# Performance work log

Hardware: AMD Instinct MI355X
Metric: run time of the kernel (lower is better)

Reference implementation:

```python
import jax, jax.numpy as jnp
import numpy as np

N_NODES = 50000
N_EDGES = 800000
BATCH = 8
IN_CH = 64
OUT_CH = 64
K = 6


def setup_inputs() -> dict:
    key = jax.random.key(0)
    k1, k2, k3, k4 = jax.random.split(key, 4)
    x = jax.random.normal(k1, (BATCH, N_NODES, IN_CH), dtype=jnp.float32)
    edge_index = jax.random.randint(k2, (2, N_EDGES), 0, N_NODES, dtype=jnp.int64)
    # small weights keep the order-K Chebyshev recursion numerically stable
    edge_weight = jax.random.normal(k3, (N_EDGES,), dtype=jnp.float32) * 0.05
    W = jax.random.normal(k4, (K, IN_CH, OUT_CH), dtype=jnp.float32) * (1.0 / np.sqrt(IN_CH))
    bias = jnp.zeros((OUT_CH,), dtype=jnp.float32)
    return {"x": x, "edge_index": edge_index, "edge_weight": edge_weight, "W": W, "bias": bias}


def _spmm(edge_index, edge_weight, x, n_nodes):
    # sparse Laplacian @ x for batched features x: [B, N, C]
    src = edge_index[1]  # gather column
    dst = edge_index[0]  # scatter row
    msg = x[:, src, :] * edge_weight[None, :, None]      # [B, E, C]
    agg = jax.ops.segment_sum(msg.transpose(1, 0, 2), dst, num_segments=n_nodes)  # [N, B, C]
    return agg.transpose(1, 0, 2)                        # [B, N, C]


def reference(x, edge_index, edge_weight, W, bias):
    n = x.shape[1]
    t_prev = x                                            # T_0
    out = jnp.einsum('bnc,co->bno', t_prev, W[0])
    if K > 1:
        t_cur = _spmm(edge_index, edge_weight, x, n)      # T_1 = L x
        out = out + jnp.einsum('bnc,co->bno', t_cur, W[1])
        for k in range(2, K):
            t_next = 2.0 * _spmm(edge_index, edge_weight, t_cur, n) - t_prev
            out = out + jnp.einsum('bnc,co->bno', t_next, W[k])
            t_prev, t_cur = t_cur, t_next
    out = out + bias
    return out
```

## Files before the change

### kernel.cpp

```cpp
#include <hip/hip_runtime.h>

#define N_NODES 50000
#define N_EDGES 800000
#define BATCH 8
#define CH 64
#define BC (BATCH * CH)
#define WSZ (CH * CH)
#define NROWS (BATCH * N_NODES)
#define TELEMS ((size_t)NROWS * CH)

typedef unsigned short u16;
typedef short bf16x8 __attribute__((ext_vector_type(8)));
typedef float f32x4 __attribute__((ext_vector_type(4)));
typedef unsigned short u16x4 __attribute__((ext_vector_type(4)));
typedef unsigned short u16x8 __attribute__((ext_vector_type(8)));

__device__ __forceinline__ u16 f2bf(float f) {
    unsigned x = __float_as_uint(f);
    return (u16)((x + 0x7fffu + ((x >> 16) & 1u)) >> 16);
}
__device__ __forceinline__ float b2f(u16 u) {
    return __uint_as_float(((unsigned)u) << 16);
}


__global__ void hist_kernel(const int* __restrict__ dst, int* __restrict__ cursor, int E) {
    int e = blockIdx.x * blockDim.x + threadIdx.x;
    if (e < E) atomicAdd(&cursor[dst[e]], 1);
}

__global__ void scan_kernel(int* cursor, int* __restrict__ row_ptr, int n) {
    const int T = 1024;
    int tid = threadIdx.x;
    int per = (n + T - 1) / T;
    int s = tid * per;
    int e = s + per; if (e > n) e = n;
    int sum = 0;
    for (int i = s; i < e; ++i) sum += cursor[i];
    __shared__ int lds[1024];
    lds[tid] = sum;
    __syncthreads();
    for (int off = 1; off < 1024; off <<= 1) {
        int t = (tid >= off) ? lds[tid - off] : 0;
        __syncthreads();
        lds[tid] += t;
        __syncthreads();
    }
    int run = lds[tid] - sum;
    for (int i = s; i < e; ++i) {
        int v = cursor[i];
        row_ptr[i] = run;
        cursor[i]  = run;
        run += v;
    }
    if (tid == T - 1) row_ptr[n] = run;
}

__global__ void scatter_kernel(const int* __restrict__ dst, const int* __restrict__ src,
                               const float* __restrict__ w, int* cursor,
                               int2* __restrict__ edges, int E) {
    int e = blockIdx.x * blockDim.x + threadIdx.x;
    if (e >= E) return;
    int d = dst[e];
    int p = atomicAdd(&cursor[d], 1);
    edges[p] = make_int2(src[e], __float_as_int(w[e]));
}

__global__ __launch_bounds__(256) void cast_x(const float* __restrict__ x, u16* __restrict__ xb) {
    size_t i = (size_t)blockIdx.x * 256 + threadIdx.x;
    f32x4 v = __builtin_nontemporal_load((const f32x4*)(x + i * 4));
    int c4 = (int)(i & 15);
    size_t bn = i >> 4;
    int b = (int)(bn / N_NODES);
    int n = (int)(bn - (size_t)b * N_NODES);
    u16x4 o;
    o.x = f2bf(v.x); o.y = f2bf(v.y); o.z = f2bf(v.z); o.w = f2bf(v.w);
    *(u16x4*)(xb + ((size_t)n * BATCH + b) * CH + c4 * 4) = o;
}

__global__ __launch_bounds__(256) void pack_w(const float* __restrict__ W, u16* __restrict__ wpack) {
    int id = blockIdx.x * 256 + threadIdx.x;
    if (id >= 48 * 64) return;
    int lane = id & 63, frag = id >> 6;
    int ct = frag & 3, cct = (frag >> 2) & 1, k = frag >> 3;
    int m = lane & 15, quad = lane >> 4;
    int c = ct * 16 + m;
#pragma unroll
    for (int j = 0; j < 8; ++j) {
        int cc = cct * 32 + quad * 8 + j;
        wpack[(size_t)id * 8 + j] = f2bf(W[k * WSZ + cc * CH + c]);
    }
}

template <bool HAS_PREV>
__global__ __launch_bounds__(256) void spmm_kernel(
        const u16* __restrict__ tcur,
        const u16* __restrict__ tprev,
        u16* __restrict__ tnext,
        const int* __restrict__ row_ptr,
        const int2* __restrict__ edges) {
    const int nwaves = gridDim.x * 4;
    const int wid = blockIdx.x * 4 + (threadIdx.x >> 6);
    const int lane = threadIdx.x & 63;
    const size_t lo = (size_t)lane * 8;

    for (int node = wid; node < N_NODES; node += nwaves) {
        float acc[8];
#pragma unroll
        for (int q = 0; q < 8; ++q) acc[q] = 0.f;

        const int beg = row_ptr[node], end = row_ptr[node + 1];
        for (int e0 = beg; e0 < end; e0 += 64) {
            int m = end - e0; if (m > 64) m = 64;
            int2 ev = edges[e0 + (lane < m ? lane : 0)];
            for (int j = 0; j < m; j += 4) {
                int   s0 = __shfl(ev.x, j);
                float w0 = __int_as_float(__shfl(ev.y, j));
                int   j1 = (j + 1 < m) ? j + 1 : j;
                int   s1 = __shfl(ev.x, j1);
                float w1 = (j + 1 < m) ? __int_as_float(__shfl(ev.y, j1)) : 0.f;
                int   j2 = (j + 2 < m) ? j + 2 : j;
                int   s2 = __shfl(ev.x, j2);
                float w2 = (j + 2 < m) ? __int_as_float(__shfl(ev.y, j2)) : 0.f;
                int   j3 = (j + 3 < m) ? j + 3 : j;
                int   s3 = __shfl(ev.x, j3);
                float w3 = (j + 3 < m) ? __int_as_float(__shfl(ev.y, j3)) : 0.f;
                u16x8 v0 = *(const u16x8*)(tcur + (size_t)s0 * BC + lo);
                u16x8 v1 = *(const u16x8*)(tcur + (size_t)s1 * BC + lo);
                u16x8 v2 = *(const u16x8*)(tcur + (size_t)s2 * BC + lo);
                u16x8 v3 = *(const u16x8*)(tcur + (size_t)s3 * BC + lo);
#pragma unroll
                for (int q = 0; q < 8; ++q) acc[q] = fmaf(w0, b2f(v0[q]), acc[q]);
#pragma unroll
                for (int q = 0; q < 8; ++q) acc[q] = fmaf(w1, b2f(v1[q]), acc[q]);
#pragma unroll
                for (int q = 0; q < 8; ++q) acc[q] = fmaf(w2, b2f(v2[q]), acc[q]);
#pragma unroll
                for (int q = 0; q < 8; ++q) acc[q] = fmaf(w3, b2f(v3[q]), acc[q]);
            }
        }

        const size_t idx = (size_t)node * BC + lo;
        u16x8 o;
        if (HAS_PREV) {
            u16x8 pv = *(const u16x8*)(tprev + idx);
#pragma unroll
            for (int q = 0; q < 8; ++q) o[q] = f2bf(2.f * acc[q] - b2f(pv[q]));
        } else {
#pragma unroll
            for (int q = 0; q < 8; ++q) o[q] = f2bf(acc[q]);
        }
        *(u16x8*)(tnext + idx) = o;
    }
}

__global__ __launch_bounds__(256) void out_gemm(
        const u16* __restrict__ tbase, size_t tstride,
        const u16* __restrict__ wpack,
        const float* __restrict__ bias,
        float* __restrict__ out, int nk, int accum) {
    const int wave = threadIdx.x >> 6, lane = threadIdx.x & 63;
    const int tile = blockIdx.x * 4 + wave;
    const int row0 = tile * 16;
    const int m = lane & 15, quad = lane >> 4;

    f32x4 acc[4];
#pragma unroll
    for (int ct = 0; ct < 4; ++ct) acc[ct] = (f32x4){0.f, 0.f, 0.f, 0.f};

    for (int k = 0; k < nk; ++k) {
        const u16* t = tbase + (size_t)k * tstride;
#pragma unroll
        for (int cct = 0; cct < 2; ++cct) {
            bf16x8 A = *(const bf16x8*)(t + (size_t)(row0 + m) * CH + cct * 32 + quad * 8);
#pragma unroll
            for (int ct = 0; ct < 4; ++ct) {
                bf16x8 B = *(const bf16x8*)(wpack + (size_t)(((k * 2 + cct) * 4 + ct) * 64 + lane) * 8);
                acc[ct] = __builtin_amdgcn_mfma_f32_16x16x32_bf16(A, B, acc[ct], 0, 0, 0);
            }
        }
    }

#pragma unroll
    for (int ct = 0; ct < 4; ++ct) {
        const int c = ct * 16 + m;
        const float bv = bias[c];
#pragma unroll
        for (int r = 0; r < 4; ++r) {
            int row = row0 + quad * 4 + r;
            float* op = out + ((size_t)(row & 7) * N_NODES + (row >> 3)) * CH + c;
            float v = acc[ct][r];
            if (accum) v += __builtin_nontemporal_load(op);
            else       v += bv;
            __builtin_nontemporal_store(v, op);
        }
    }
}

extern "C" void kernel_launch(void* const* d_in, const int* in_sizes, int n_in,
                              void* d_out, int out_size, void* d_ws, size_t ws_size,
                              hipStream_t stream) {
    const float* x    = (const float*)d_in[0];
    const int*   ei   = (const int*)d_in[1];
    const float* ew   = (const float*)d_in[2];
    const float* W    = (const float*)d_in[3];
    const float* bias = (const float*)d_in[4];
    float* out = (float*)d_out;

    const int* dst = ei;
    const int* src = ei + N_EDGES;

    const size_t SB = TELEMS * sizeof(u16);
    const size_t EXTRA = 2 * 200192 + (size_t)N_EDGES * sizeof(int2) + 49664;
    const size_t NEED_PRIMARY = 6 * SB + EXTRA;
    const bool primary = (ws_size >= NEED_PRIMARY);
    const int nbuf = primary ? 6 : 3;

    char* ws = (char*)d_ws;
    size_t off = 0;
    u16* tbase = (u16*)(ws + off); off += (size_t)nbuf * SB;
    int* row_ptr = (int*)(ws + off); off += 200192;
    int* cursor  = (int*)(ws + off); off += 200192;
    int2* edges  = (int2*)(ws + off); off += (size_t)N_EDGES * sizeof(int2);
    u16* wpack   = (u16*)(ws + off); off += 49664;
    (void)off; (void)n_in; (void)in_sizes; (void)out_size;

    (void)hipMemsetAsync(cursor, 0, (size_t)N_NODES * sizeof(int), stream);
    hist_kernel<<<(N_EDGES + 255) / 256, 256, 0, stream>>>(dst, cursor, N_EDGES);
    scan_kernel<<<1, 1024, 0, stream>>>(cursor, row_ptr, N_NODES);
    scatter_kernel<<<(N_EDGES + 255) / 256, 256, 0, stream>>>(dst, src, ew, cursor,
                                                              edges, N_EDGES);
    cast_x<<<(int)(TELEMS / 4 / 256), 256, 0, stream>>>(x, tbase);
    pack_w<<<12, 256, 0, stream>>>(W, wpack);

    const int SPMM_GRID = 2048;
    u16* t0 = tbase;
    if (primary) {
        u16* t1 = tbase + 1 * TELEMS;
        u16* t2 = tbase + 2 * TELEMS;
        u16* t3 = tbase + 3 * TELEMS;
        u16* t4 = tbase + 4 * TELEMS;
        u16* t5 = tbase + 5 * TELEMS;
        spmm_kernel<false><<<SPMM_GRID, 256, 0, stream>>>(t0, nullptr, t1, row_ptr, edges);
        spmm_kernel<true ><<<SPMM_GRID, 256, 0, stream>>>(t1, t0, t2, row_ptr, edges);
        spmm_kernel<true ><<<SPMM_GRID, 256, 0, stream>>>(t2, t1, t3, row_ptr, edges);
        spmm_kernel<true ><<<SPMM_GRID, 256, 0, stream>>>(t3, t2, t4, row_ptr, edges);
        spmm_kernel<true ><<<SPMM_GRID, 256, 0, stream>>>(t4, t3, t5, row_ptr, edges);
        out_gemm<<<NROWS / 16 / 4, 256, 0, stream>>>(tbase, TELEMS, wpack, bias, out, 6, 0);
    } else {
        u16* t1 = tbase + 1 * TELEMS;
        u16* t2 = tbase + 2 * TELEMS;
        const int GG = NROWS / 16 / 4;
        spmm_kernel<false><<<SPMM_GRID, 256, 0, stream>>>(t0, nullptr, t1, row_ptr, edges);
        out_gemm<<<GG, 256, 0, stream>>>(t0, TELEMS, wpack, bias, out, 2, 0);
        spmm_kernel<true ><<<SPMM_GRID, 256, 0, stream>>>(t1, t0, t2, row_ptr, edges);
        out_gemm<<<GG, 256, 0, stream>>>(t2, TELEMS, wpack + 2 * WSZ, bias, out, 1, 1);
        spmm_kernel<true ><<<SPMM_GRID, 256, 0, stream>>>(t2, t1, t0, row_ptr, edges);
        out_gemm<<<GG, 256, 0, stream>>>(t0, TELEMS, wpack + 3 * WSZ, bias, out, 1, 1);
        spmm_kernel<true ><<<SPMM_GRID, 256, 0, stream>>>(t0, t2, t1, row_ptr, edges);
        out_gemm<<<GG, 256, 0, stream>>>(t1, TELEMS, wpack + 4 * WSZ, bias, out, 1, 1);
        spmm_kernel<true ><<<SPMM_GRID, 256, 0, stream>>>(t1, t0, t2, row_ptr, edges);
        out_gemm<<<GG, 256, 0, stream>>>(t2, TELEMS, wpack + 5 * WSZ, bias, out, 1, 1);
    }
}
```

Baseline: 1.099 ms.

## Merge preprocessing kernels and launch one wave per node in SpMM

The histogram kernel now also does the x cast, and the scatter kernel now also packs W, so the preprocessing chain issues fewer kernel launches. The SpMM kernel drops its grid-stride loop and launches N_NODES/4 blocks with one wave per node. It also splits the edge loop into a full 4-wide body plus a scalar tail, which removes the clamped-index and conditional-weight logic. The costs are more blocks to schedule and no reuse of a wave across nodes, which could cost some latency hiding.

```diff
diff --git a/kernel.cpp b/kernel.cpp
--- a/kernel.cpp
+++ b/kernel.cpp
@@ -8,6 +8,9 @@
 #define WSZ (CH * CH)
 #define NROWS (BATCH * N_NODES)
 #define TELEMS ((size_t)NROWS * CH)
+#define HIST_BLOCKS ((N_EDGES + 255) / 256)
+#define CAST_BLOCKS ((int)(TELEMS / 4 / 256))
+#define PACK_BLOCKS 12
 
 typedef unsigned short u16;
 typedef short bf16x8 __attribute__((ext_vector_type(8)));
@@ -24,9 +27,24 @@
 }
 
 
-__global__ void hist_kernel(const int* __restrict__ dst, int* __restrict__ cursor, int E) {
-    int e = blockIdx.x * blockDim.x + threadIdx.x;
-    if (e < E) atomicAdd(&cursor[dst[e]], 1);
+__global__ __launch_bounds__(256) void hist_cast_kernel(
+        const int* __restrict__ dst, int* __restrict__ cursor,
+        const float* __restrict__ x, u16* __restrict__ xb) {
+    int bid = blockIdx.x;
+    if (bid < HIST_BLOCKS) {
+        int e = bid * 256 + threadIdx.x;
+        if (e < N_EDGES) atomicAdd(&cursor[dst[e]], 1);
+        return;
+    }
+    size_t i = (size_t)(bid - HIST_BLOCKS) * 256 + threadIdx.x;
+    f32x4 v = __builtin_nontemporal_load((const f32x4*)(x + i * 4));
+    int c4 = (int)(i & 15);
+    size_t bn = i >> 4;
+    int b = (int)(bn / N_NODES);
+    int n = (int)(bn - (size_t)b * N_NODES);
+    u16x4 o;
+    o.x = f2bf(v.x); o.y = f2bf(v.y); o.z = f2bf(v.z); o.w = f2bf(v.w);
+    *(u16x4*)(xb + ((size_t)n * BATCH + b) * CH + c4 * 4) = o;
 }
 
 __global__ void scan_kernel(int* cursor, int* __restrict__ row_ptr, int n) {
@@ -56,30 +74,20 @@
     if (tid == T - 1) row_ptr[n] = run;
 }
 
-__global__ void scatter_kernel(const int* __restrict__ dst, const int* __restrict__ src,
-                               const float* __restrict__ w, int* cursor,
-                               int2* __restrict__ edges, int E) {
-    int e = blockIdx.x * blockDim.x + threadIdx.x;
-    if (e >= E) return;
-    int d = dst[e];
-    int p = atomicAdd(&cursor[d], 1);
-    edges[p] = make_int2(src[e], __float_as_int(w[e]));
-}
-
-__global__ __launch_bounds__(256) void cast_x(const float* __restrict__ x, u16* __restrict__ xb) {
-    size_t i = (size_t)blockIdx.x * 256 + threadIdx.x;
-    f32x4 v = __builtin_nontemporal_load((const f32x4*)(x + i * 4));
-    int c4 = (int)(i & 15);
-    size_t bn = i >> 4;
-    int b = (int)(bn / N_NODES);
-    int n = (int)(bn - (size_t)b * N_NODES);
-    u16x4 o;
-    o.x = f2bf(v.x); o.y = f2bf(v.y); o.z = f2bf(v.z); o.w = f2bf(v.w);
-    *(u16x4*)(xb + ((size_t)n * BATCH + b) * CH + c4 * 4) = o;
-}
-
-__global__ __launch_bounds__(256) void pack_w(const float* __restrict__ W, u16* __restrict__ wpack) {
-    int id = blockIdx.x * 256 + threadIdx.x;
+__global__ __launch_bounds__(256) void scatter_pack_kernel(
+        const int* __restrict__ dst, const int* __restrict__ src,
+        const float* __restrict__ w, int* cursor, int2* __restrict__ edges,
+        const float* __restrict__ W, u16* __restrict__ wpack) {
+    int bid = blockIdx.x;
+    if (bid < HIST_BLOCKS) {
+        int e = bid * 256 + threadIdx.x;
+        if (e >= N_EDGES) return;
+        int d = dst[e];
+        int p = atomicAdd(&cursor[d], 1);
+        edges[p] = make_int2(src[e], __float_as_int(w[e]));
+        return;
+    }
+    int id = (bid - HIST_BLOCKS) * 256 + threadIdx.x;
     if (id >= 48 * 64) return;
     int lane = id & 63, frag = id >> 6;
     int ct = frag & 3, cct = (frag >> 2) & 1, k = frag >> 3;
@@ -99,59 +107,61 @@
         u16* __restrict__ tnext,
         const int* __restrict__ row_ptr,
         const int2* __restrict__ edges) {
-    const int nwaves = gridDim.x * 4;
-    const int wid = blockIdx.x * 4 + (threadIdx.x >> 6);
+    const int node = blockIdx.x * 4 + (threadIdx.x >> 6);
     const int lane = threadIdx.x & 63;
     const size_t lo = (size_t)lane * 8;
 
-    for (int node = wid; node < N_NODES; node += nwaves) {
-        float acc[8];
-#pragma unroll
-        for (int q = 0; q < 8; ++q) acc[q] = 0.f;
-
-        const int beg = row_ptr[node], end = row_ptr[node + 1];
-        for (int e0 = beg; e0 < end; e0 += 64) {
-            int m = end - e0; if (m > 64) m = 64;
-            int2 ev = edges[e0 + (lane < m ? lane : 0)];
-            for (int j = 0; j < m; j += 4) {
-                int   s0 = __shfl(ev.x, j);
-                float w0 = __int_as_float(__shfl(ev.y, j));
-                int   j1 = (j + 1 < m) ? j + 1 : j;
-                int   s1 = __shfl(ev.x, j1);
-                float w1 = (j + 1 < m) ? __int_as_float(__shfl(ev.y, j1)) : 0.f;
-                int   j2 = (j + 2 < m) ? j + 2 : j;
-                int   s2 = __shfl(ev.x, j2);
-                float w2 = (j + 2 < m) ? __int_as_float(__shfl(ev.y, j2)) : 0.f;
-                int   j3 = (j + 3 < m) ? j + 3 : j;
-                int   s3 = __shfl(ev.x, j3);
-                float w3 = (j + 3 < m) ? __int_as_float(__shfl(ev.y, j3)) : 0.f;
-                u16x8 v0 = *(const u16x8*)(tcur + (size_t)s0 * BC + lo);
-                u16x8 v1 = *(const u16x8*)(tcur + (size_t)s1 * BC + lo);
-                u16x8 v2 = *(const u16x8*)(tcur + (size_t)s2 * BC + lo);
-                u16x8 v3 = *(const u16x8*)(tcur + (size_t)s3 * BC + lo);
-#pragma unroll
-                for (int q = 0; q < 8; ++q) acc[q] = fmaf(w0, b2f(v0[q]), acc[q]);
-#pragma unroll
-                for (int q = 0; q < 8; ++q) acc[q] = fmaf(w1, b2f(v1[q]), acc[q]);
-#pragma unroll
-                for (int q = 0; q < 8; ++q) acc[q] = fmaf(w2, b2f(v2[q]), acc[q]);
-#pragma unroll
-                for (int q = 0; q < 8; ++q) acc[q] = fmaf(w3, b2f(v3[q]), acc[q]);
-            }
-        }
-
-        const size_t idx = (size_t)node * BC + lo;
-        u16x8 o;
-        if (HAS_PREV) {
-            u16x8 pv = *(const u16x8*)(tprev + idx);
-#pragma unroll
-            for (int q = 0; q < 8; ++q) o[q] = f2bf(2.f * acc[q] - b2f(pv[q]));
-        } else {
-#pragma unroll
-            for (int q = 0; q < 8; ++q) o[q] = f2bf(acc[q]);
-        }
-        *(u16x8*)(tnext + idx) = o;
-    }
+    float acc[8];
+#pragma unroll
+    for (int q = 0; q < 8; ++q) acc[q] = 0.f;
+
+    const int beg = row_ptr[node], end = row_ptr[node + 1];
+    for (int e0 = beg; e0 < end; e0 += 64) {
+        int m = end - e0; if (m > 64) m = 64;
+        int2 ev = edges[e0 + (lane < m ? lane : 0)];
+        int j = 0;
+        for (; j + 4 <= m; j += 4) {
+            int   s0 = __shfl(ev.x, j);
+            int   s1 = __shfl(ev.x, j + 1);
+            int   s2 = __shfl(ev.x, j + 2);
+            int   s3 = __shfl(ev.x, j + 3);
+            float w0 = __int_as_float(__shfl(ev.y, j));
+            float w1 = __int_as_float(__shfl(ev.y, j + 1));
+            float w2 = __int_as_float(__shfl(ev.y, j + 2));
+            float w3 = __int_as_float(__shfl(ev.y, j + 3));
+            u16x8 v0 = *(const u16x8*)(tcur + (size_t)s0 * BC + lo);
+            u16x8 v1 = *(const u16x8*)(tcur + (size_t)s1 * BC + lo);
+            u16x8 v2 = *(const u16x8*)(tcur + (size_t)s2 * BC + lo);
+            u16x8 v3 = *(const u16x8*)(tcur + (size_t)s3 * BC + lo);
+#pragma unroll
+            for (int q = 0; q < 8; ++q) acc[q] = fmaf(w0, b2f(v0[q]), acc[q]);
+#pragma unroll
+            for (int q = 0; q < 8; ++q) acc[q] = fmaf(w1, b2f(v1[q]), acc[q]);
+#pragma unroll
+            for (int q = 0; q < 8; ++q) acc[q] = fmaf(w2, b2f(v2[q]), acc[q]);
+#pragma unroll
+            for (int q = 0; q < 8; ++q) acc[q] = fmaf(w3, b2f(v3[q]), acc[q]);
+        }
+        for (; j < m; ++j) {
+            int   s = __shfl(ev.x, j);
+            float w = __int_as_float(__shfl(ev.y, j));
+            u16x8 v = *(const u16x8*)(tcur + (size_t)s * BC + lo);
+#pragma unroll
+            for (int q = 0; q < 8; ++q) acc[q] = fmaf(w, b2f(v[q]), acc[q]);
+        }
+    }
+
+    const size_t idx = (size_t)node * BC + lo;
+    u16x8 o;
+    if (HAS_PREV) {
+        u16x8 pv = *(const u16x8*)(tprev + idx);
+#pragma unroll
+        for (int q = 0; q < 8; ++q) o[q] = f2bf(2.f * acc[q] - b2f(pv[q]));
+    } else {
+#pragma unroll
+        for (int q = 0; q < 8; ++q) o[q] = f2bf(acc[q]);
+    }
+    *(u16x8*)(tnext + idx) = o;
 }
 
 __global__ __launch_bounds__(256) void out_gemm(
@@ -226,14 +236,12 @@
     (void)off; (void)n_in; (void)in_sizes; (void)out_size;
 
     (void)hipMemsetAsync(cursor, 0, (size_t)N_NODES * sizeof(int), stream);
-    hist_kernel<<<(N_EDGES + 255) / 256, 256, 0, stream>>>(dst, cursor, N_EDGES);
+    hist_cast_kernel<<<HIST_BLOCKS + CAST_BLOCKS, 256, 0, stream>>>(dst, cursor, x, tbase);
     scan_kernel<<<1, 1024, 0, stream>>>(cursor, row_ptr, N_NODES);
-    scatter_kernel<<<(N_EDGES + 255) / 256, 256, 0, stream>>>(dst, src, ew, cursor,
-                                                              edges, N_EDGES);
-    cast_x<<<(int)(TELEMS / 4 / 256), 256, 0, stream>>>(x, tbase);
-    pack_w<<<12, 256, 0, stream>>>(W, wpack);
-
-    const int SPMM_GRID = 2048;
+    scatter_pack_kernel<<<HIST_BLOCKS + PACK_BLOCKS, 256, 0, stream>>>(dst, src, ew, cursor,
+                                                                       edges, W, wpack);
+
+    const int SPMM_GRID = N_NODES / 4;
     u16* t0 = tbase;
     if (primary) {
         u16* t1 = tbase + 1 * TELEMS;
```

Measured after the change: 1.068 ms. -2.8%, faster.
